# Optimization experiments

Hardware: AMD Instinct MI355X
Metric: run time of the kernel (lower is better)

Reference implementation:

```python
import jax, jax.numpy as jnp
import numpy as np
from jax import lax

NKP = 21  # hand keypoints
CH = 32   # channel width forced by K.dot(g, W) with W:[input_ch, output_dim]
OUT_DIM = 32


def setup_inputs() -> dict:
    key = jax.random.key(0)
    ks = jax.random.split(key, 9)
    B, H, W = 8, 96, 96
    s = 0.05
    return {
        "x": jax.random.normal(ks[0], (B, H, W, CH), dtype=jnp.float32),
        # shared 1x1 conv (conv2): 1x1 conv == matmul over channels
        "w2": jax.random.normal(ks[1], (CH, CH), dtype=jnp.float32) * s,
        "b2": jnp.zeros((CH,), dtype=jnp.float32),
        # per-keypoint effective 1x1 conv (conv2a over concat of identical f blocks
        # collapses exactly to a 32->32 kernel = sum of per-block slices)
        "wa": jax.random.normal(ks[2], (NKP, CH, CH), dtype=jnp.float32) * s,
        "ba": jnp.zeros((NKP, CH), dtype=jnp.float32),
        # per-keypoint 3x3 conv (conv2b), HWIO layout
        "wb": jax.random.normal(ks[3], (NKP, 3, 3, CH, CH), dtype=jnp.float32) * s,
        "bb": jnp.zeros((NKP, CH), dtype=jnp.float32),
        # per-keypoint learned projection W_i : [CH, output_dim]
        "Wp": jax.random.normal(ks[4], (NKP, CH, OUT_DIM), dtype=jnp.float32) * s,
    }


def _conv3x3(h, w, b):
    # h: [B,H,W,C], w: [3,3,C,C]
    y = lax.conv_general_dilated(h, w, (1, 1), "SAME",
                                 dimension_numbers=("NHWC", "HWIO", "NHWC"))
    return jax.nn.relu(y + b)


def reference(x, w2, b2, wa, ba, wb, bb, Wp):
    f = jax.nn.relu(jnp.einsum("bhwc,cd->bhwd", x, w2) + b2)          # [B,H,W,32]
    # per-keypoint 1x1 conv on concat([f, f_j...]) == effective 32->32 1x1 conv
    h = jax.nn.relu(jnp.einsum("bhwc,ncd->nbhwd", f, wa)
                    + ba[:, None, None, None, :])                      # [21,B,H,W,32]
    g = jax.vmap(_conv3x3)(h, wb, bb)                                  # [21,B,H,W,32]
    # sum over output_dim of (g @ W_i) == g @ W_i.sum(-1)
    lsum = jnp.einsum("nbhwc,nc->nbhw", g, Wp.sum(axis=-1))            # [21,B,H,W]
    fn = f.sum(axis=-1)[None] + lsum                                   # [21,B,H,W]
    return jnp.moveaxis(fn, 0, -1)                                     # [B,H,W,21]
```

## Files before the change

kernel.cpp:

```cpp
#include <hip/hip_runtime.h>

#define BATCH 8
#define IMH 96
#define IMW 96
#define CH 32
#define NKP 21
#define TILE 16
#define HALO 18
#define FPITCH 40
#define NPIX 324
#define NPIX_PAD 336
#define NGRP 3

typedef __bf16 bf16x8 __attribute__((ext_vector_type(8)));
typedef __bf16 bf16x4 __attribute__((ext_vector_type(4)));
typedef float  f32x4  __attribute__((ext_vector_type(4)));

static __device__ inline f32x4 mfma16(bf16x8 a, bf16x8 b, f32x4 c) {
    return __builtin_amdgcn_mfma_f32_16x16x32_bf16(a, b, c, 0, 0, 0);
}

__global__ void __launch_bounds__(256)
f_precompute_kernel(const float* __restrict__ x,
                    const float* __restrict__ w2, const float* __restrict__ b2,
                    __bf16* __restrict__ fout, float* __restrict__ fsum_out)
{
    const int gp = blockIdx.x * 256 + threadIdx.x;
    const float* xp = x + (size_t)gp * CH;
    float xv[CH];
    #pragma unroll
    for (int e = 0; e < CH; e += 4) {
        float4 v = *(const float4*)(xp + e);
        xv[e] = v.x; xv[e+1] = v.y; xv[e+2] = v.z; xv[e+3] = v.w;
    }
    float f[CH];
    #pragma unroll
    for (int c = 0; c < CH; ++c) f[c] = b2[c];
    #pragma unroll
    for (int e = 0; e < CH; ++e) {
        const float xe = xv[e];
        const float* wr = w2 + e * CH;
        #pragma unroll
        for (int c = 0; c < CH; ++c) f[c] = fmaf(xe, wr[c], f[c]);
    }
    float fs = 0.f;
    #pragma unroll
    for (int c = 0; c < CH; ++c) { f[c] = fmaxf(f[c], 0.f); fs += f[c]; }
    #pragma unroll
    for (int q = 0; q < 4; ++q) {
        bf16x8 v;
        #pragma unroll
        for (int j = 0; j < 8; ++j) v[j] = (__bf16)f[q * 8 + j];
        *(bf16x8*)&fout[(size_t)gp * CH + q * 8] = v;
    }
    fsum_out[gp] = fs;
}

__global__ void __launch_bounds__(64)
wprep_kernel(const float* __restrict__ wa, const float* __restrict__ wb,
             const float* __restrict__ Wp,
             __bf16* __restrict__ wfrag, float* __restrict__ wv)
{
    const int n = blockIdx.x;
    const int lane = threadIdx.x;
    const int r4 = lane & 15, kb = (lane >> 4) * 8;

    const float* wan = wa + n * CH * CH;
    #pragma unroll
    for (int hf = 0; hf < 2; ++hf) {
        bf16x8 v;
        #pragma unroll
        for (int j = 0; j < 8; ++j)
            v[j] = (__bf16)wan[(kb + j) * CH + hf * 16 + r4];
        *(bf16x8*)&wfrag[(((size_t)n * 20 + hf) * 64 + lane) * 8] = v;
    }
    const float* wbn = wb + (size_t)n * 9 * CH * CH;
    for (int t = 0; t < 9; ++t)
        #pragma unroll
        for (int hf = 0; hf < 2; ++hf) {
            bf16x8 v;
            #pragma unroll
            for (int j = 0; j < 8; ++j)
                v[j] = (__bf16)wbn[(t * CH + kb + j) * CH + hf * 16 + r4];
            *(bf16x8*)&wfrag[(((size_t)n * 20 + 2 + t * 2 + hf) * 64 + lane) * 8] = v;
        }
    if (lane < CH) {
        const float* wp = Wp + (n * CH + lane) * CH;
        float s = 0.f;
        #pragma unroll
        for (int d = 0; d < CH; ++d) s += wp[d];
        wv[n * CH + lane] = s;
    }
}

__global__ void __launch_bounds__(256, 3)
ckp_mfma2_kernel(const __bf16* __restrict__ fws, const float* __restrict__ fsum_ws,
                 const __bf16* __restrict__ wfrag, const float* __restrict__ wvws,
                 const float* __restrict__ ba, const float* __restrict__ bb,
                 float* __restrict__ out)
{
    __shared__ __bf16 sF[NPIX_PAD * FPITCH];
    __shared__ __bf16 sH[NPIX_PAD * FPITCH];
    __shared__ float  sFsum[TILE * TILE];

    const int tid  = threadIdx.x;
    const int tile = blockIdx.x;
    const int b    = blockIdx.y;
    const int ty0  = (tile / (IMW / TILE)) * TILE;
    const int tx0  = (tile % (IMW / TILE)) * TILE;

    const int lane = tid & 63;
    const int w    = tid >> 6;
    const int r4   = lane & 15;
    const int g16  = lane >> 4;
    const int kb   = g16 * 8;
    const int kb4  = g16 * 4;

    for (int i = tid; i < NPIX * 4; i += 256) {
        const int p = i >> 2, q = i & 3;
        const int hy = p / HALO, hx = p % HALO;
        const int Y = ty0 + hy - 1, X = tx0 + hx - 1;
        bf16x8 v;
        if (Y >= 0 && Y < IMH && X >= 0 && X < IMW) {
            v = *(const bf16x8*)&fws[(((size_t)b * IMH + Y) * IMW + X) * CH + q * 8];
        } else {
            #pragma unroll
            for (int j = 0; j < 8; ++j) v[j] = (__bf16)0.f;
        }
        *(bf16x8*)&sF[p * FPITCH + q * 8] = v;
    }
    if (tid < 48) {
        bf16x8 z;
        #pragma unroll
        for (int j = 0; j < 8; ++j) z[j] = (__bf16)0.f;
        *(bf16x8*)&sF[(NPIX + (tid >> 2)) * FPITCH + (tid & 3) * 8] = z;
    }
    {
        const int iy = tid >> 4, ix = tid & 15;
        sFsum[tid] = fsum_ws[((size_t)b * IMH + ty0 + iy) * IMW + tx0 + ix];
    }
    __syncthreads();

    for (int ni = 0; ni < NGRP; ++ni) {
        const int n = blockIdx.z * NGRP + ni;
        const __bf16* wf = wfrag + (size_t)n * 20 * 64 * 8;

        bf16x8 wafr0 = *(const bf16x8*)&wf[((size_t)0 * 64 + lane) * 8];
        bf16x8 wafr1 = *(const bf16x8*)&wf[((size_t)1 * 64 + lane) * 8];
        bf16x8 wbfr[9][2];
        #pragma unroll
        for (int t = 0; t < 9; ++t)
            #pragma unroll
            for (int hf = 0; hf < 2; ++hf)
                wbfr[t][hf] = *(const bf16x8*)&wf[((size_t)(2 + t * 2 + hf) * 64 + lane) * 8];

        const f32x4 ba0 = *(const f32x4*)&ba[n * CH + kb4];
        const f32x4 ba1 = *(const f32x4*)&ba[n * CH + 16 + kb4];
        const f32x4 bb0 = *(const f32x4*)&bb[n * CH + kb4];
        const f32x4 bb1 = *(const f32x4*)&bb[n * CH + 16 + kb4];
        const f32x4 wv0 = *(const f32x4*)&wvws[n * CH + kb4];
        const f32x4 wv1 = *(const f32x4*)&wvws[n * CH + 16 + kb4];

        if (ni) __syncthreads();

        for (int t = w; t < 21; t += 4) {
            const int p = t * 16 + r4;
            bf16x8 ffr = *(const bf16x8*)&sF[p * FPITCH + kb];
            f32x4 a0 = {0.f, 0.f, 0.f, 0.f};
            f32x4 a1 = {0.f, 0.f, 0.f, 0.f};
            a0 = mfma16(wafr0, ffr, a0);
            a1 = mfma16(wafr1, ffr, a1);
            bf16x4 h0, h1;
            #pragma unroll
            for (int r = 0; r < 4; ++r) {
                h0[r] = (__bf16)fmaxf(a0[r] + ba0[r], 0.f);
                h1[r] = (__bf16)fmaxf(a1[r] + ba1[r], 0.f);
            }
            *(bf16x4*)&sH[p * FPITCH + kb4]      = h0;
            *(bf16x4*)&sH[p * FPITCH + 16 + kb4] = h1;
        }
        __syncthreads();

        const int w4 = w * 4;
        f32x4 acc[4][2];
        #pragma unroll
        for (int ai = 0; ai < 4; ++ai) {
            acc[ai][0] = (f32x4){0.f, 0.f, 0.f, 0.f};
            acc[ai][1] = (f32x4){0.f, 0.f, 0.f, 0.f};
        }
        #pragma unroll
        for (int dx = 0; dx < 3; ++dx) {
            #pragma unroll
            for (int k = 0; k < 6; ++k) {
                const int hy = w4 + k;
                bf16x8 hfr = *(const bf16x8*)&sH[(hy * HALO + r4 + dx) * FPITCH + kb];
                #pragma unroll
                for (int dy = 0; dy < 3; ++dy) {
                    const int ai = k - dy;
                    if (ai >= 0 && ai < 4) {
                        acc[ai][0] = mfma16(wbfr[dy * 3 + dx][0], hfr, acc[ai][0]);
                        acc[ai][1] = mfma16(wbfr[dy * 3 + dx][1], hfr, acc[ai][1]);
                    }
                }
            }
        }

        #pragma unroll
        for (int ai = 0; ai < 4; ++ai) {
            float s = 0.f;
            #pragma unroll
            for (int r = 0; r < 4; ++r) {
                s += fmaxf(acc[ai][0][r] + bb0[r], 0.f) * wv0[r];
                s += fmaxf(acc[ai][1][r] + bb1[r], 0.f) * wv1[r];
            }
            s += __shfl_xor(s, 16);
            s += __shfl_xor(s, 32);
            if (g16 == 0) {
                const int oy = w4 + ai;
                out[(((size_t)b * IMH + ty0 + oy) * IMW + tx0 + r4) * NKP + n]
                    = s + sFsum[oy * TILE + r4];
            }
        }
    }
}

#define PITCH 33
__global__ void __launch_bounds__(256)
ckp_fused_kernel(const float* __restrict__ x,
                 const float* __restrict__ w2, const float* __restrict__ b2,
                 const float* __restrict__ wa, const float* __restrict__ ba,
                 const float* __restrict__ wb, const float* __restrict__ bb,
                 const float* __restrict__ Wp,
                 float* __restrict__ out)
{
    __shared__ float sH[HALO * HALO * PITCH];
    __shared__ float sFsum[TILE * TILE];
    __shared__ float sWv[CH];

    const int tid  = threadIdx.x;
    const int tile = blockIdx.x;
    const int b    = blockIdx.y;
    const int n    = blockIdx.z;
    const int ty0  = (tile / (IMW / TILE)) * TILE;
    const int tx0  = (tile % (IMW / TILE)) * TILE;

    if (tid < CH) {
        const float* wp = Wp + (n * CH + tid) * CH;
        float s = 0.f;
        #pragma unroll
        for (int d = 0; d < CH; ++d) s += wp[d];
        sWv[tid] = s;
    }
    const float* wan = wa + n * CH * CH;
    const float* ban = ba + n * CH;

    for (int p = tid; p < HALO * HALO; p += 256) {
        const int hy = p / HALO, hx = p % HALO;
        const int Y = ty0 + hy - 1, X = tx0 + hx - 1;
        float* dst = &sH[p * PITCH];
        if (Y >= 0 && Y < IMH && X >= 0 && X < IMW) {
            const float* xp = x + (((size_t)b * IMH + Y) * IMW + X) * CH;
            float xv[CH];
            #pragma unroll
            for (int e = 0; e < CH; e += 4) {
                float4 v = *(const float4*)(xp + e);
                xv[e] = v.x; xv[e+1] = v.y; xv[e+2] = v.z; xv[e+3] = v.w;
            }
            float f[CH];
            #pragma unroll
            for (int c = 0; c < CH; ++c) f[c] = b2[c];
            #pragma unroll
            for (int e = 0; e < CH; ++e) {
                const float xe = xv[e];
                const float* wr = w2 + e * CH;
                #pragma unroll
                for (int c = 0; c < CH; ++c) f[c] = fmaf(xe, wr[c], f[c]);
            }
            float fs = 0.f;
            #pragma unroll
            for (int c = 0; c < CH; ++c) { f[c] = fmaxf(f[c], 0.f); fs += f[c]; }
            if (hy >= 1 && hy <= TILE && hx >= 1 && hx <= TILE)
                sFsum[(hy - 1) * TILE + (hx - 1)] = fs;
            float h[CH];
            #pragma unroll
            for (int c = 0; c < CH; ++c) h[c] = ban[c];
            #pragma unroll
            for (int e = 0; e < CH; ++e) {
                const float fe = f[e];
                const float* wr = wan + e * CH;
                #pragma unroll
                for (int c = 0; c < CH; ++c) h[c] = fmaf(fe, wr[c], h[c]);
            }
            #pragma unroll
            for (int c = 0; c < CH; ++c) dst[c] = fmaxf(h[c], 0.f);
        } else {
            #pragma unroll
            for (int c = 0; c < CH; ++c) dst[c] = 0.f;
        }
    }
    __syncthreads();

    const int iy = tid / TILE, ix = tid % TILE;
    const float* wbn = wb + n * 9 * CH * CH;
    const float* bbn = bb + n * CH;
    float g[CH];
    #pragma unroll
    for (int c = 0; c < CH; ++c) g[c] = bbn[c];
    for (int dy = 0; dy < 3; ++dy) {
        for (int dx = 0; dx < 3; ++dx) {
            const float* hrow = &sH[((iy + dy) * HALO + (ix + dx)) * PITCH];
            const float* wr0 = wbn + (dy * 3 + dx) * CH * CH;
            #pragma unroll
            for (int e = 0; e < CH; ++e) {
                const float hv = hrow[e];
                const float* wr = wr0 + e * CH;
                #pragma unroll
                for (int c = 0; c < CH; ++c) g[c] = fmaf(hv, wr[c], g[c]);
            }
        }
    }
    float lsum = 0.f;
    #pragma unroll
    for (int c = 0; c < CH; ++c) lsum = fmaf(fmaxf(g[c], 0.f), sWv[c], lsum);
    const int Y = ty0 + iy, X = tx0 + ix;
    out[(((size_t)b * IMH + Y) * IMW + X) * NKP + n] = sFsum[tid] + lsum;
}

extern "C" void kernel_launch(void* const* d_in, const int* in_sizes, int n_in,
                              void* d_out, int out_size, void* d_ws, size_t ws_size,
                              hipStream_t stream) {
    const float* x  = (const float*)d_in[0];
    const float* w2 = (const float*)d_in[1];
    const float* b2 = (const float*)d_in[2];
    const float* wa = (const float*)d_in[3];
    const float* ba = (const float*)d_in[4];
    const float* wb = (const float*)d_in[5];
    const float* bb = (const float*)d_in[6];
    const float* Wp = (const float*)d_in[7];
    float* out = (float*)d_out;

    const size_t npix     = (size_t)BATCH * IMH * IMW;
    const size_t f_bytes  = npix * CH * sizeof(__bf16);
    const size_t fs_bytes = npix * sizeof(float);
    const size_t wf_bytes = (size_t)NKP * 20 * 64 * 8 * sizeof(__bf16);
    const size_t wv_bytes = (size_t)NKP * CH * sizeof(float);
    const size_t need = f_bytes + fs_bytes + wf_bytes + wv_bytes;

    if (ws_size >= need) {
        __bf16* f_ws    = (__bf16*)d_ws;
        float*  fsum_ws = (float*)((char*)d_ws + f_bytes);
        __bf16* wf_ws   = (__bf16*)((char*)d_ws + f_bytes + fs_bytes);
        float*  wv_ws   = (float*)((char*)d_ws + f_bytes + fs_bytes + wf_bytes);

        f_precompute_kernel<<<dim3(npix / 256), dim3(256), 0, stream>>>(x, w2, b2, f_ws, fsum_ws);
        wprep_kernel<<<dim3(NKP), dim3(64), 0, stream>>>(wa, wb, Wp, wf_ws, wv_ws);
        dim3 grid((IMH / TILE) * (IMW / TILE), BATCH, NKP / NGRP);
        ckp_mfma2_kernel<<<grid, dim3(256), 0, stream>>>(f_ws, fsum_ws, wf_ws, wv_ws, ba, bb, out);
    } else {
        dim3 grid((IMH / TILE) * (IMW / TILE), BATCH, NKP);
        ckp_fused_kernel<<<grid, dim3(256), 0, stream>>>(x, w2, b2, wa, ba, wb, bb, Wp, out);
    }
}
```

Before: 66.85 us.

## Merge prep kernels and stream f tile directly from global into 1x1 MFMA

Folds the f precompute and weight-fragment prep into one launch to save a kernel launch. The main kernel drops the shared-memory staging of the f halo tile and the fsum tile. Each wave now loads its f fragments straight from global memory with precomputed clamped offsets and a validity mask, and reads fsum from global at output time. The 3x3 weight fragments are loaded per dx column instead of all 18 up front, cutting register pressure so the launch bound can rise to 4 blocks per SM. The trade-off is that each of the three keypoint iterations re-reads the f halo from global/L2 instead of reading it from LDS.

```diff
diff --git a/kernel.cpp b/kernel.cpp
--- a/kernel.cpp
+++ b/kernel.cpp
@@ -11,6 +11,7 @@
 #define NPIX 324
 #define NPIX_PAD 336
 #define NGRP 3
+#define FBLK 1152
 
 typedef __bf16 bf16x8 __attribute__((ext_vector_type(8)));
 typedef __bf16 bf16x4 __attribute__((ext_vector_type(4)));
@@ -20,88 +21,85 @@
     return __builtin_amdgcn_mfma_f32_16x16x32_bf16(a, b, c, 0, 0, 0);
 }
 
-__global__ void __launch_bounds__(256)
-f_precompute_kernel(const float* __restrict__ x,
-                    const float* __restrict__ w2, const float* __restrict__ b2,
-                    __bf16* __restrict__ fout, float* __restrict__ fsum_out)
+__global__ void __launch_bounds__(64)
+prep_kernel(const float* __restrict__ x,
+            const float* __restrict__ w2, const float* __restrict__ b2,
+            const float* __restrict__ wa, const float* __restrict__ wb,
+            const float* __restrict__ Wp,
+            __bf16* __restrict__ fout, float* __restrict__ fsum_out,
+            __bf16* __restrict__ wfrag, float* __restrict__ wv)
 {
-    const int gp = blockIdx.x * 256 + threadIdx.x;
-    const float* xp = x + (size_t)gp * CH;
-    float xv[CH];
-    #pragma unroll
-    for (int e = 0; e < CH; e += 4) {
-        float4 v = *(const float4*)(xp + e);
-        xv[e] = v.x; xv[e+1] = v.y; xv[e+2] = v.z; xv[e+3] = v.w;
-    }
-    float f[CH];
-    #pragma unroll
-    for (int c = 0; c < CH; ++c) f[c] = b2[c];
-    #pragma unroll
-    for (int e = 0; e < CH; ++e) {
-        const float xe = xv[e];
-        const float* wr = w2 + e * CH;
-        #pragma unroll
-        for (int c = 0; c < CH; ++c) f[c] = fmaf(xe, wr[c], f[c]);
-    }
-    float fs = 0.f;
-    #pragma unroll
-    for (int c = 0; c < CH; ++c) { f[c] = fmaxf(f[c], 0.f); fs += f[c]; }
-    #pragma unroll
-    for (int q = 0; q < 4; ++q) {
-        bf16x8 v;
-        #pragma unroll
-        for (int j = 0; j < 8; ++j) v[j] = (__bf16)f[q * 8 + j];
-        *(bf16x8*)&fout[(size_t)gp * CH + q * 8] = v;
-    }
-    fsum_out[gp] = fs;
-}
-
-__global__ void __launch_bounds__(64)
-wprep_kernel(const float* __restrict__ wa, const float* __restrict__ wb,
-             const float* __restrict__ Wp,
-             __bf16* __restrict__ wfrag, float* __restrict__ wv)
-{
-    const int n = blockIdx.x;
+    const int bx = blockIdx.x;
     const int lane = threadIdx.x;
-    const int r4 = lane & 15, kb = (lane >> 4) * 8;
-
-    const float* wan = wa + n * CH * CH;
-    #pragma unroll
-    for (int hf = 0; hf < 2; ++hf) {
-        bf16x8 v;
-        #pragma unroll
-        for (int j = 0; j < 8; ++j)
-            v[j] = (__bf16)wan[(kb + j) * CH + hf * 16 + r4];
-        *(bf16x8*)&wfrag[(((size_t)n * 20 + hf) * 64 + lane) * 8] = v;
-    }
-    const float* wbn = wb + (size_t)n * 9 * CH * CH;
-    for (int t = 0; t < 9; ++t)
+    if (bx < FBLK) {
+        const int gp = bx * 64 + lane;
+        const float* xp = x + (size_t)gp * CH;
+        float xv[CH];
+        #pragma unroll
+        for (int e = 0; e < CH; e += 4) {
+            float4 v = *(const float4*)(xp + e);
+            xv[e] = v.x; xv[e+1] = v.y; xv[e+2] = v.z; xv[e+3] = v.w;
+        }
+        float f[CH];
+        #pragma unroll
+        for (int c = 0; c < CH; ++c) f[c] = b2[c];
+        #pragma unroll
+        for (int e = 0; e < CH; ++e) {
+            const float xe = xv[e];
+            const float* wr = w2 + e * CH;
+            #pragma unroll
+            for (int c = 0; c < CH; ++c) f[c] = fmaf(xe, wr[c], f[c]);
+        }
+        float fs = 0.f;
+        #pragma unroll
+        for (int c = 0; c < CH; ++c) { f[c] = fmaxf(f[c], 0.f); fs += f[c]; }
+        #pragma unroll
+        for (int q = 0; q < 4; ++q) {
+            bf16x8 v;
+            #pragma unroll
+            for (int j = 0; j < 8; ++j) v[j] = (__bf16)f[q * 8 + j];
+            *(bf16x8*)&fout[(size_t)gp * CH + q * 8] = v;
+        }
+        fsum_out[gp] = fs;
+    } else {
+        const int n = bx - FBLK;
+        const int r4 = lane & 15, kb = (lane >> 4) * 8;
+        const float* wan = wa + n * CH * CH;
         #pragma unroll
         for (int hf = 0; hf < 2; ++hf) {
             bf16x8 v;
             #pragma unroll
             for (int j = 0; j < 8; ++j)
-                v[j] = (__bf16)wbn[(t * CH + kb + j) * CH + hf * 16 + r4];
-            *(bf16x8*)&wfrag[(((size_t)n * 20 + 2 + t * 2 + hf) * 64 + lane) * 8] = v;
-        }
-    if (lane < CH) {
-        const float* wp = Wp + (n * CH + lane) * CH;
-        float s = 0.f;
-        #pragma unroll
-        for (int d = 0; d < CH; ++d) s += wp[d];
-        wv[n * CH + lane] = s;
-    }
-}
-
-__global__ void __launch_bounds__(256, 3)
-ckp_mfma2_kernel(const __bf16* __restrict__ fws, const float* __restrict__ fsum_ws,
+                v[j] = (__bf16)wan[(kb + j) * CH + hf * 16 + r4];
+            *(bf16x8*)&wfrag[(((size_t)n * 20 + hf) * 64 + lane) * 8] = v;
+        }
+        const float* wbn = wb + (size_t)n * 9 * CH * CH;
+        for (int t = 0; t < 9; ++t)
+            #pragma unroll
+            for (int hf = 0; hf < 2; ++hf) {
+                bf16x8 v;
+                #pragma unroll
+                for (int j = 0; j < 8; ++j)
+                    v[j] = (__bf16)wbn[(t * CH + kb + j) * CH + hf * 16 + r4];
+                *(bf16x8*)&wfrag[(((size_t)n * 20 + 2 + t * 2 + hf) * 64 + lane) * 8] = v;
+            }
+        if (lane < CH) {
+            const float* wp = Wp + (n * CH + lane) * CH;
+            float s = 0.f;
+            #pragma unroll
+            for (int d = 0; d < CH; ++d) s += wp[d];
+            wv[n * CH + lane] = s;
+        }
+    }
+}
+
+__global__ void __launch_bounds__(256, 4)
+ckp_mfma4_kernel(const __bf16* __restrict__ fws, const float* __restrict__ fsum_ws,
                  const __bf16* __restrict__ wfrag, const float* __restrict__ wvws,
                  const float* __restrict__ ba, const float* __restrict__ bb,
                  float* __restrict__ out)
 {
-    __shared__ __bf16 sF[NPIX_PAD * FPITCH];
     __shared__ __bf16 sH[NPIX_PAD * FPITCH];
-    __shared__ float  sFsum[TILE * TILE];
 
     const int tid  = threadIdx.x;
     const int tile = blockIdx.x;
@@ -115,96 +113,89 @@
     const int g16  = lane >> 4;
     const int kb   = g16 * 8;
     const int kb4  = g16 * 4;
-
-    for (int i = tid; i < NPIX * 4; i += 256) {
-        const int p = i >> 2, q = i & 3;
+    const int w4   = w * 4;
+
+    int voff[6]; unsigned dmask = 0;
+    #pragma unroll
+    for (int i = 0; i < 6; ++i) {
+        const int t  = w + 4 * i;
+        const int p  = t * 16 + r4;
         const int hy = p / HALO, hx = p % HALO;
-        const int Y = ty0 + hy - 1, X = tx0 + hx - 1;
-        bf16x8 v;
-        if (Y >= 0 && Y < IMH && X >= 0 && X < IMW) {
-            v = *(const bf16x8*)&fws[(((size_t)b * IMH + Y) * IMW + X) * CH + q * 8];
-        } else {
-            #pragma unroll
-            for (int j = 0; j < 8; ++j) v[j] = (__bf16)0.f;
-        }
-        *(bf16x8*)&sF[p * FPITCH + q * 8] = v;
-    }
-    if (tid < 48) {
-        bf16x8 z;
-        #pragma unroll
-        for (int j = 0; j < 8; ++j) z[j] = (__bf16)0.f;
-        *(bf16x8*)&sF[(NPIX + (tid >> 2)) * FPITCH + (tid & 3) * 8] = z;
-    }
-    {
-        const int iy = tid >> 4, ix = tid & 15;
-        sFsum[tid] = fsum_ws[((size_t)b * IMH + ty0 + iy) * IMW + tx0 + ix];
-    }
-    __syncthreads();
+        const int Y  = ty0 + hy - 1, X = tx0 + hx - 1;
+        const bool dv = (t <= 20) & (hy < HALO) & (Y >= 0) & (Y < IMH) & (X >= 0) & (X < IMW);
+        const int Yc = min(max(Y, 0), IMH - 1), Xc = min(max(X, 0), IMW - 1);
+        voff[i] = ((b * IMH + Yc) * IMW + Xc) * CH + kb;
+        dmask |= (dv ? 1u : 0u) << i;
+    }
 
     for (int ni = 0; ni < NGRP; ++ni) {
         const int n = blockIdx.z * NGRP + ni;
         const __bf16* wf = wfrag + (size_t)n * 20 * 64 * 8;
-
         bf16x8 wafr0 = *(const bf16x8*)&wf[((size_t)0 * 64 + lane) * 8];
         bf16x8 wafr1 = *(const bf16x8*)&wf[((size_t)1 * 64 + lane) * 8];
-        bf16x8 wbfr[9][2];
-        #pragma unroll
-        for (int t = 0; t < 9; ++t)
-            #pragma unroll
-            for (int hf = 0; hf < 2; ++hf)
-                wbfr[t][hf] = *(const bf16x8*)&wf[((size_t)(2 + t * 2 + hf) * 64 + lane) * 8];
-
         const f32x4 ba0 = *(const f32x4*)&ba[n * CH + kb4];
         const f32x4 ba1 = *(const f32x4*)&ba[n * CH + 16 + kb4];
+
+        if (ni) __syncthreads();
+
+        #pragma unroll
+        for (int i = 0; i < 6; ++i) {
+            const int t = w + 4 * i;
+            if (t <= 20) {
+                bf16x8 v = *(const bf16x8*)&fws[voff[i]];
+                const bool dv = (dmask >> i) & 1;
+                if (!dv) {
+                    #pragma unroll
+                    for (int j = 0; j < 8; ++j) v[j] = (__bf16)0.f;
+                }
+                const f32x4 z = {0.f, 0.f, 0.f, 0.f};
+                f32x4 a0 = mfma16(wafr0, v, z);
+                f32x4 a1 = mfma16(wafr1, v, z);
+                const int p = t * 16 + r4;
+                bf16x4 h0, h1;
+                #pragma unroll
+                for (int r = 0; r < 4; ++r) {
+                    h0[r] = dv ? (__bf16)fmaxf(a0[r] + ba0[r], 0.f) : (__bf16)0.f;
+                    h1[r] = dv ? (__bf16)fmaxf(a1[r] + ba1[r], 0.f) : (__bf16)0.f;
+                }
+                *(bf16x4*)&sH[p * FPITCH + kb4]      = h0;
+                *(bf16x4*)&sH[p * FPITCH + 16 + kb4] = h1;
+            }
+        }
+        __syncthreads();
+
+        f32x4 acc[4][2];
+        #pragma unroll
+        for (int ai = 0; ai < 4; ++ai) {
+            acc[ai][0] = (f32x4){0.f, 0.f, 0.f, 0.f};
+            acc[ai][1] = (f32x4){0.f, 0.f, 0.f, 0.f};
+        }
+        #pragma unroll
+        for (int dx = 0; dx < 3; ++dx) {
+            bf16x8 wt[3][2];
+            #pragma unroll
+            for (int dy = 0; dy < 3; ++dy)
+                #pragma unroll
+                for (int hf = 0; hf < 2; ++hf)
+                    wt[dy][hf] = *(const bf16x8*)&wf[((size_t)(2 + (dy * 3 + dx) * 2 + hf) * 64 + lane) * 8];
+            #pragma unroll
+            for (int k = 0; k < 6; ++k) {
+                bf16x8 hfr = *(const bf16x8*)&sH[((w4 + k) * HALO + r4 + dx) * FPITCH + kb];
+                #pragma unroll
+                for (int dy = 0; dy < 3; ++dy) {
+                    const int ai = k - dy;
+                    if (ai >= 0 && ai < 4) {
+                        acc[ai][0] = mfma16(wt[dy][0], hfr, acc[ai][0]);
+                        acc[ai][1] = mfma16(wt[dy][1], hfr, acc[ai][1]);
+                    }
+                }
+            }
+        }
+
         const f32x4 bb0 = *(const f32x4*)&bb[n * CH + kb4];
         const f32x4 bb1 = *(const f32x4*)&bb[n * CH + 16 + kb4];
         const f32x4 wv0 = *(const f32x4*)&wvws[n * CH + kb4];
         const f32x4 wv1 = *(const f32x4*)&wvws[n * CH + 16 + kb4];
-
-        if (ni) __syncthreads();
-
-        for (int t = w; t < 21; t += 4) {
-            const int p = t * 16 + r4;
-            bf16x8 ffr = *(const bf16x8*)&sF[p * FPITCH + kb];
-            f32x4 a0 = {0.f, 0.f, 0.f, 0.f};
-            f32x4 a1 = {0.f, 0.f, 0.f, 0.f};
-            a0 = mfma16(wafr0, ffr, a0);
-            a1 = mfma16(wafr1, ffr, a1);
-            bf16x4 h0, h1;
-            #pragma unroll
-            for (int r = 0; r < 4; ++r) {
-                h0[r] = (__bf16)fmaxf(a0[r] + ba0[r], 0.f);
-                h1[r] = (__bf16)fmaxf(a1[r] + ba1[r], 0.f);
-            }
-            *(bf16x4*)&sH[p * FPITCH + kb4]      = h0;
-            *(bf16x4*)&sH[p * FPITCH + 16 + kb4] = h1;
-        }
-        __syncthreads();
-
-        const int w4 = w * 4;
-        f32x4 acc[4][2];
-        #pragma unroll
-        for (int ai = 0; ai < 4; ++ai) {
-            acc[ai][0] = (f32x4){0.f, 0.f, 0.f, 0.f};
-            acc[ai][1] = (f32x4){0.f, 0.f, 0.f, 0.f};
-        }
-        #pragma unroll
-        for (int dx = 0; dx < 3; ++dx) {
-            #pragma unroll
-            for (int k = 0; k < 6; ++k) {
-                const int hy = w4 + k;
-                bf16x8 hfr = *(const bf16x8*)&sH[(hy * HALO + r4 + dx) * FPITCH + kb];
-                #pragma unroll
-                for (int dy = 0; dy < 3; ++dy) {
-                    const int ai = k - dy;
-                    if (ai >= 0 && ai < 4) {
-                        acc[ai][0] = mfma16(wbfr[dy * 3 + dx][0], hfr, acc[ai][0]);
-                        acc[ai][1] = mfma16(wbfr[dy * 3 + dx][1], hfr, acc[ai][1]);
-                    }
-                }
-            }
-        }
-
         #pragma unroll
         for (int ai = 0; ai < 4; ++ai) {
             float s = 0.f;
@@ -216,9 +207,8 @@
             s += __shfl_xor(s, 16);
             s += __shfl_xor(s, 32);
             if (g16 == 0) {
-                const int oy = w4 + ai;
-                out[(((size_t)b * IMH + ty0 + oy) * IMW + tx0 + r4) * NKP + n]
-                    = s + sFsum[oy * TILE + r4];
+                const int gp = (b * IMH + ty0 + w4 + ai) * IMW + tx0 + r4;
+                out[(size_t)gp * NKP + n] = s + fsum_ws[gp];
             }
         }
     }
@@ -352,10 +342,10 @@
         __bf16* wf_ws   = (__bf16*)((char*)d_ws + f_bytes + fs_bytes);
         float*  wv_ws   = (float*)((char*)d_ws + f_bytes + fs_bytes + wf_bytes);
 
-        f_precompute_kernel<<<dim3(npix / 256), dim3(256), 0, stream>>>(x, w2, b2, f_ws, fsum_ws);
-        wprep_kernel<<<dim3(NKP), dim3(64), 0, stream>>>(wa, wb, Wp, wf_ws, wv_ws);
+        prep_kernel<<<dim3(FBLK + NKP), dim3(64), 0, stream>>>(
+            x, w2, b2, wa, wb, Wp, f_ws, fsum_ws, wf_ws, wv_ws);
         dim3 grid((IMH / TILE) * (IMW / TILE), BATCH, NKP / NGRP);
-        ckp_mfma2_kernel<<<grid, dim3(256), 0, stream>>>(f_ws, fsum_ws, wf_ws, wv_ws, ba, bb, out);
+        ckp_mfma4_kernel<<<grid, dim3(256), 0, stream>>>(f_ws, fsum_ws, wf_ws, wv_ws, ba, bb, out);
     } else {
         dim3 grid((IMH / TILE) * (IMW / TILE), BATCH, NKP);
         ckp_fused_kernel<<<grid, dim3(256), 0, stream>>>(x, w2, b2, wa, ba, wb, bb, Wp, out);
```

Measured after the change: 54.42 us, median of 2. 18.6% less time.
